# Optimization experiments

Hardware: AMD Instinct MI355X
Metric: run time of the kernel (lower is better)

Reference implementation:

```python
import jax, jax.numpy as jnp
import numpy as np

B, C_IN, L = 16, 64, 1024
HID, OUT, ORDER = 1024, 512, 4
EPS = 1e-5


def setup_inputs() -> dict:
    key = jax.random.key(0)
    ks = jax.random.split(key, 4)
    return {
        "x": jax.random.normal(ks[0], (B, C_IN, L), jnp.float32),
        "W_in": jax.random.normal(ks[1], (C_IN, HID), jnp.float32) / np.sqrt(C_IN).astype(np.float32),
        "b_in": jnp.zeros((HID,), jnp.float32),
        "coeffs1": jax.random.normal(ks[2], (HID, HID, ORDER), jnp.float32) * 0.01,
        "bias1": jnp.zeros((HID,), jnp.float32),
        "g1": jnp.ones((HID,), jnp.float32),
        "beta1": jnp.zeros((HID,), jnp.float32),
        "coeffs2": jax.random.normal(ks[3], (OUT, HID, ORDER), jnp.float32) * 0.01,
        "bias2": jnp.zeros((OUT,), jnp.float32),
        "g2": jnp.ones((OUT,), jnp.float32),
        "beta2": jnp.zeros((OUT,), jnp.float32),
    }


def _taylor_kan(x, coeffs, bias):
    # x: (B, L, C_in); coeffs: (out, C_in, order); y[b,l,o] = sum_i sum_c x^i * coeffs[o,c,i]
    # Expressed as order-wise GEMMs with a running power -- no (B,out,L,C) expand.
    order = coeffs.shape[-1]
    y = jnp.zeros(x.shape[:2] + (coeffs.shape[0],), x.dtype)
    xp = jnp.ones_like(x)  # x**0 (matches torch 0**0 == 1)
    for i in range(order):
        y = y + jnp.einsum('blc,oc->blo', xp, coeffs[:, :, i])
        if i + 1 < order:
            xp = xp * x
    return y + bias


def _layernorm(x, g, b):
    mu = jnp.mean(x, -1, keepdims=True)
    var = jnp.mean((x - mu) ** 2, -1, keepdims=True)
    return (x - mu) * jax.lax.rsqrt(var + EPS) * g + b


def reference(x, W_in, b_in, coeffs1, bias1, g1, beta1, coeffs2, bias2, g2, beta2):
    # x: (B, C_in, L) -> project channels to hidden: (B, L, HID)
    h = jnp.einsum('bcl,ch->blh', x, W_in) + b_in
    h = _taylor_kan(h, coeffs1, bias1)            # (B, L, HID)
    h = jax.nn.gelu(_layernorm(h, g1, beta1), approximate=False)
    h = _taylor_kan(h, coeffs2, bias2)            # (B, L, OUT)
    h = _layernorm(h, g2, beta2)
    return jnp.mean(h, axis=1)                    # adaptive avg pool over L -> (B, OUT)
```

## Files before the change

### kernel.cpp

```cpp
#include <hip/hip_runtime.h>
#include <math.h>

#define Bsz  16
#define CIN  64
#define LEN  1024
#define HIDN 1024
#define OUTN 512
#define MTOT (Bsz*LEN)
#define KTOT (3*HIDN)
#define LCHUNKS 32
#define LROWS   (LEN/LCHUNKS)

typedef __attribute__((ext_vector_type(8))) short bf16x8;
typedef __attribute__((ext_vector_type(16))) float f32x16;

__device__ __forceinline__ unsigned short f2bf(float x) {
    union { float f; unsigned int u; } v; v.f = x;
    unsigned int r = v.u + 0x7fff + ((v.u >> 16) & 1);
    return (unsigned short)(r >> 16);
}
__device__ __forceinline__ float bf2f(unsigned short u) {
    union { unsigned int u; float f; } v; v.u = ((unsigned int)u) << 16;
    return v.f;
}
__device__ __forceinline__ void gload_lds16(const void* g, void* l) {
    __builtin_amdgcn_global_load_lds((const __attribute__((address_space(1))) void*)g,
                                     (__attribute__((address_space(3))) void*)l, 16, 0, 0);
}

__global__ __launch_bounds__(256) void prep_all(const float* __restrict__ coeffs1,
                                                const float* __restrict__ bias1,
                                                const float* __restrict__ coeffs2,
                                                const float* __restrict__ bias2,
                                                const float* __restrict__ x,
                                                const float* __restrict__ Win,
                                                unsigned short* __restrict__ W1T,
                                                float* __restrict__ b1e,
                                                unsigned short* __restrict__ W2T,
                                                float* __restrict__ b2e,
                                                unsigned short* __restrict__ xT,
                                                unsigned short* __restrict__ WinT) {
    __shared__ float sm[64 * 65];
    int bid = blockIdx.x, t = threadIdx.x;
    if (bid < 1536) {
        const float* coeffs; const float* bias; unsigned short* WT; float* beff; int o;
        if (bid < 1024) { coeffs = coeffs1; bias = bias1; WT = W1T; beff = b1e; o = bid; }
        else            { coeffs = coeffs2; bias = bias2; WT = W2T; beff = b2e; o = bid - 1024; }
        float s = 0.f;
        unsigned short* wrow = WT + (size_t)o * KTOT;
        for (int c = t; c < HIDN; c += 256) {
            float4 v = *(const float4*)(coeffs + ((size_t)o * HIDN + c) * 4);
            s += v.x;
            wrow[c]            = f2bf(v.y);
            wrow[HIDN + c]     = f2bf(v.z);
            wrow[2 * HIDN + c] = f2bf(v.w);
        }
        for (int off = 32; off > 0; off >>= 1) s += __shfl_down(s, off, 64);
        if ((t & 63) == 0) sm[t >> 6] = s;
        __syncthreads();
        if (t == 0) beff[o] = bias[o] + sm[0] + sm[1] + sm[2] + sm[3];
    } else {
        const float* src; unsigned short* dstbase; size_t src_rstride;
        int c0;
        if (bid < 1792) {
            int tile = bid - 1536; int b = tile >> 4; c0 = (tile & 15) * 64;
            src = x + (size_t)b * CIN * LEN;  src_rstride = LEN;
            dstbase = xT + ((size_t)b * LEN + c0) * CIN;
        } else {
            int tile = bid - 1792; c0 = tile * 64;
            src = Win; src_rstride = HIDN;
            dstbase = WinT + (size_t)c0 * CIN;
        }
#pragma unroll
        for (int it = 0; it < 4; it++) {
            int idx = t + it * 256;
            int c = idx >> 4, q = idx & 15;
            float4 v = *(const float4*)(src + (size_t)c * src_rstride + c0 + q * 4);
            sm[c * 65 + q * 4 + 0] = v.x;
            sm[c * 65 + q * 4 + 1] = v.y;
            sm[c * 65 + q * 4 + 2] = v.z;
            sm[c * 65 + q * 4 + 3] = v.w;
        }
        __syncthreads();
        int ll = t >> 2, cg = (t & 3) * 16;
        unsigned short* dst = dstbase + (size_t)ll * CIN + cg;
#pragma unroll
        for (int j = 0; j < 4; j++) {
            int c = cg + j * 4;
            ushort4 w = { f2bf(sm[(c + 0) * 65 + ll]), f2bf(sm[(c + 1) * 65 + ll]),
                          f2bf(sm[(c + 2) * 65 + ll]), f2bf(sm[(c + 3) * 65 + ll]) };
            *(ushort4*)(dst + j * 4) = w;
        }
    }
}

__global__ __launch_bounds__(256) void proj_mfma(const unsigned short* __restrict__ xT,
                                                 const unsigned short* __restrict__ WinT,
                                                 const float* __restrict__ bin,
                                                 unsigned short* __restrict__ Hpow) {
    __shared__ unsigned short smem[2 * 128 * 64];
    unsigned short* As = smem;
    unsigned short* Bs = smem + 128 * 64;
    unsigned short* ht = smem;
    int t = threadIdx.x, lane = t & 63, wave = t >> 6;
    int m0 = blockIdx.x * 128, n0 = blockIdx.y * 128;
    int srow = lane >> 3, sgcc = (lane & 7) ^ srow;
    const unsigned short* Ab = xT + (size_t)m0 * CIN;
    const unsigned short* Bb = WinT + (size_t)n0 * CIN;

    f32x16 acc[2][2] = {};
    int wr = (wave >> 1) * 64, wc = (wave & 1) * 64;
    int row32 = lane & 31, half = lane >> 5;

#pragma unroll
    for (int j = 0; j < 4; j++) {
        int rgrp = wave * 32 + j * 8;
        gload_lds16(Ab + (size_t)(rgrp + srow) * CIN + sgcc * 8, As + rgrp * 64);
        gload_lds16(Bb + (size_t)(rgrp + srow) * CIN + sgcc * 8, Bs + rgrp * 64);
    }
    __syncthreads();
#pragma unroll
    for (int ks = 0; ks < 4; ks++) {
        int cidx = ks * 2 + half;
        bf16x8 af[2], bf[2];
#pragma unroll
        for (int mt = 0; mt < 2; mt++) {
            int r = wr + mt * 32 + row32;
            af[mt] = *(const bf16x8*)(As + r * 64 + ((cidx ^ (r & 7)) << 3));
        }
#pragma unroll
        for (int nt = 0; nt < 2; nt++) {
            int c = wc + nt * 32 + row32;
            bf[nt] = *(const bf16x8*)(Bs + c * 64 + ((cidx ^ (c & 7)) << 3));
        }
#pragma unroll
        for (int mt = 0; mt < 2; mt++)
#pragma unroll
            for (int nt = 0; nt < 2; nt++)
                acc[mt][nt] = __builtin_amdgcn_mfma_f32_32x32x16_bf16(af[mt], bf[nt], acc[mt][nt], 0, 0, 0);
    }
    __syncthreads();
#pragma unroll
    for (int nt = 0; nt < 2; nt++) {
        int ocl = wc + nt * 32 + row32;
        float bo = bin[n0 + ocl];
#pragma unroll
        for (int mt = 0; mt < 2; mt++) {
#pragma unroll
            for (int reg = 0; reg < 16; reg++) {
                int rl = wr + mt * 32 + (reg & 3) + 8 * (reg >> 2) + 4 * half;
                ht[rl * 128 + ocl] = f2bf(acc[mt][nt][reg] + bo);
            }
        }
    }
    __syncthreads();
#pragma unroll
    for (int p = 0; p < 8; p++) {
        int r = p * 16 + (t >> 4);
        int c = (t & 15) * 8;
        bf16x8 hv = *(const bf16x8*)(ht + r * 128 + c);
        bf16x8 h2v, h3v;
#pragma unroll
        for (int j = 0; j < 8; j++) {
            float f = bf2f((unsigned short)hv[j]);
            float f2 = f * f;
            h2v[j] = (short)f2bf(f2);
            h3v[j] = (short)f2bf(f2 * f);
        }
        unsigned short* d = Hpow + (size_t)(m0 + r) * KTOT + n0 + c;
        *(bf16x8*)(d)            = hv;
        *(bf16x8*)(d + HIDN)     = h2v;
        *(bf16x8*)(d + 2 * HIDN) = h3v;
    }
}

template<int N, bool BF16OUT>
__global__ __launch_bounds__(256) void mfma_gemm(const unsigned short* __restrict__ A,
                                                 const unsigned short* __restrict__ BT,
                                                 const float* __restrict__ beff,
                                                 void* __restrict__ Yv) {
    __shared__ unsigned short As[128 * 64];
    __shared__ unsigned short Bs[128 * 64];
    int t = threadIdx.x;
    int lane = t & 63, wave = t >> 6;
    int m0 = blockIdx.x * 128, n0 = blockIdx.y * 128;
    const unsigned short* Ab = A + (size_t)m0 * KTOT;
    const unsigned short* Bb = BT + (size_t)n0 * KTOT;

    int srow = lane >> 3;
    int sgcc = (lane & 7) ^ srow;

    f32x16 acc[2][2] = {};
    int wr = (wave >> 1) * 64;
    int wc = (wave & 1) * 64;
    int row32 = lane & 31, half = lane >> 5;

    for (int k0 = 0; k0 < KTOT; k0 += 64) {
#pragma unroll
        for (int j = 0; j < 4; j++) {
            int rgrp = wave * 32 + j * 8;
            gload_lds16(Ab + ((size_t)(rgrp + srow) * KTOT + k0 + sgcc * 8), As + rgrp * 64);
            gload_lds16(Bb + ((size_t)(rgrp + srow) * KTOT + k0 + sgcc * 8), Bs + rgrp * 64);
        }
        __syncthreads();
#pragma unroll
        for (int ks = 0; ks < 4; ks++) {
            int cidx = ks * 2 + half;
            bf16x8 af[2], bf[2];
#pragma unroll
            for (int mt = 0; mt < 2; mt++) {
                int r = wr + mt * 32 + row32;
                af[mt] = *(const bf16x8*)(As + r * 64 + ((cidx ^ (r & 7)) << 3));
            }
#pragma unroll
            for (int nt = 0; nt < 2; nt++) {
                int c = wc + nt * 32 + row32;
                bf[nt] = *(const bf16x8*)(Bs + c * 64 + ((cidx ^ (c & 7)) << 3));
            }
#pragma unroll
            for (int mt = 0; mt < 2; mt++)
#pragma unroll
                for (int nt = 0; nt < 2; nt++)
                    acc[mt][nt] = __builtin_amdgcn_mfma_f32_32x32x16_bf16(af[mt], bf[nt], acc[mt][nt], 0, 0, 0);
        }
        __syncthreads();
    }
#pragma unroll
    for (int nt = 0; nt < 2; nt++) {
        int oc = n0 + wc + nt * 32 + row32;
        float bo = beff[oc];
#pragma unroll
        for (int mt = 0; mt < 2; mt++) {
#pragma unroll
            for (int reg = 0; reg < 16; reg++) {
                int rl = (reg & 3) + 8 * (reg >> 2) + 4 * half;
                int mr = m0 + wr + mt * 32 + rl;
                float v = acc[mt][nt][reg] + bo;
                if (BF16OUT) ((unsigned short*)Yv)[(size_t)mr * N + oc] = f2bf(v);
                else         ((float*)Yv)[(size_t)mr * N + oc] = v;
            }
        }
    }
}

__global__ __launch_bounds__(256) void ln_gelu(const unsigned short* __restrict__ y1,
                                               const float* __restrict__ g,
                                               const float* __restrict__ be,
                                               unsigned short* __restrict__ Gpow) {
    __shared__ float2 red[2][2];
    int t = threadIdx.x;
    int rhalf = t >> 7, l = t & 127, wid = (t >> 6) & 1;
    int m = blockIdx.x * 2 + rhalf;
    bf16x8 u = *(const bf16x8*)(y1 + (size_t)m * HIDN + l * 8);
    float v[8];
    float s = 0.f, ss = 0.f;
#pragma unroll
    for (int j = 0; j < 8; j++) {
        v[j] = bf2f((unsigned short)u[j]);
        s += v[j]; ss += v[j] * v[j];
    }
    for (int off = 32; off > 0; off >>= 1) {
        s  += __shfl_down(s, off, 64);
        ss += __shfl_down(ss, off, 64);
    }
    if ((t & 63) == 0) red[rhalf][wid] = make_float2(s, ss);
    __syncthreads();
    float sT  = red[rhalf][0].x + red[rhalf][1].x;
    float ssT = red[rhalf][0].y + red[rhalf][1].y;
    float mu = sT * (1.f / HIDN);
    float var = ssT * (1.f / HIDN) - mu * mu;
    float rs = rsqrtf(var + 1e-5f);
    float4 gA = *(const float4*)(g + l * 8),  gB = *(const float4*)(g + l * 8 + 4);
    float4 bA = *(const float4*)(be + l * 8), bB = *(const float4*)(be + l * 8 + 4);
    float gv[8] = { gA.x, gA.y, gA.z, gA.w, gB.x, gB.y, gB.z, gB.w };
    float bv[8] = { bA.x, bA.y, bA.z, bA.w, bB.x, bB.y, bB.z, bB.w };
    bf16x8 p1, p2, p3;
#pragma unroll
    for (int j = 0; j < 8; j++) {
        float xn = (v[j] - mu) * rs * gv[j] + bv[j];
        float gl = xn * 0.5f * (1.f + erff(xn * 0.70710678118654752f));
        float g2 = gl * gl;
        p1[j] = (short)f2bf(gl);
        p2[j] = (short)f2bf(g2);
        p3[j] = (short)f2bf(g2 * gl);
    }
    unsigned short* dst = Gpow + (size_t)m * KTOT + l * 8;
    *(bf16x8*)(dst)            = p1;
    *(bf16x8*)(dst + HIDN)     = p2;
    *(bf16x8*)(dst + 2 * HIDN) = p3;
}

__global__ __launch_bounds__(256) void ln_pool_partial(const unsigned short* __restrict__ y2,
                                                       const float* __restrict__ g,
                                                       const float* __restrict__ be,
                                                       float* __restrict__ partial) {
    __shared__ float part[4][OUTN];
    int t = threadIdx.x, lane = t & 63, wave = t >> 6;
    int b = blockIdx.x, chunk = blockIdx.y;
    int mbase = b * LEN + chunk * LROWS;

    float4 gA = *(const float4*)(g + 8 * lane),  gB = *(const float4*)(g + 8 * lane + 4);
    float4 bA = *(const float4*)(be + 8 * lane), bB = *(const float4*)(be + 8 * lane + 4);
    float gv[8] = { gA.x, gA.y, gA.z, gA.w, gB.x, gB.y, gB.z, gB.w };
    float bv[8] = { bA.x, bA.y, bA.z, bA.w, bB.x, bB.y, bB.z, bB.w };

    float acc[8] = {0.f, 0.f, 0.f, 0.f, 0.f, 0.f, 0.f, 0.f};
    for (int rr = wave; rr < LROWS; rr += 4) {
        bf16x8 u = *(const bf16x8*)(y2 + (size_t)(mbase + rr) * OUTN + 8 * lane);
        float v[8];
        float s = 0.f, ss = 0.f;
#pragma unroll
        for (int j = 0; j < 8; j++) {
            v[j] = bf2f((unsigned short)u[j]);
            s += v[j]; ss += v[j] * v[j];
        }
        for (int off = 32; off > 0; off >>= 1) {
            s  += __shfl_down(s, off, 64);
            ss += __shfl_down(ss, off, 64);
        }
        s  = __shfl(s, 0, 64);
        ss = __shfl(ss, 0, 64);
        float mu = s * (1.f / OUTN);
        float var = ss * (1.f / OUTN) - mu * mu;
        float rs = rsqrtf(var + 1e-5f);
#pragma unroll
        for (int j = 0; j < 8; j++)
            acc[j] += (v[j] - mu) * rs * gv[j] + bv[j];
    }
    *(float4*)(&part[wave][8 * lane])     = *(float4*)(&acc[0]);
    *(float4*)(&part[wave][8 * lane + 4]) = *(float4*)(&acc[4]);
    __syncthreads();
    float p0 = part[0][2*t] + part[1][2*t] + part[2][2*t] + part[3][2*t];
    float p1 = part[0][2*t+1] + part[1][2*t+1] + part[2][2*t+1] + part[3][2*t+1];
    float* dst = partial + ((size_t)b * LCHUNKS + chunk) * OUTN;
    *(float2*)(dst + 2 * t) = make_float2(p0, p1);
}

__global__ __launch_bounds__(256) void pool_reduce(const float* __restrict__ partial,
                                                   float* __restrict__ out) {
    int b = blockIdx.x, t = threadIdx.x;
    const float* src = partial + (size_t)b * LCHUNKS * OUTN;
    float s0 = 0.f, s1 = 0.f;
    for (int c = 0; c < LCHUNKS; c++) {
        float2 v = *(const float2*)(src + (size_t)c * OUTN + 2 * t);
        s0 += v.x; s1 += v.y;
    }
    *(float2*)(out + (size_t)b * OUTN + 2 * t) = make_float2(s0 * (1.f / LEN), s1 * (1.f / LEN));
}

extern "C" void kernel_launch(void* const* d_in, const int* in_sizes, int n_in,
                              void* d_out, int out_size, void* d_ws, size_t ws_size,
                              hipStream_t stream) {
    const float* x       = (const float*)d_in[0];
    const float* Win     = (const float*)d_in[1];
    const float* bin     = (const float*)d_in[2];
    const float* coeffs1 = (const float*)d_in[3];
    const float* bias1   = (const float*)d_in[4];
    const float* g1      = (const float*)d_in[5];
    const float* beta1   = (const float*)d_in[6];
    const float* coeffs2 = (const float*)d_in[7];
    const float* bias2   = (const float*)d_in[8];
    const float* g2      = (const float*)d_in[9];
    const float* beta2   = (const float*)d_in[10];
    float* out = (float*)d_out;

    char* ws = (char*)d_ws;
    unsigned short* Hpow = (unsigned short*)ws;
    char* p1 = ws + (size_t)MTOT * KTOT * 2;
    unsigned short* y1   = (unsigned short*)p1;
    unsigned short* y2   = (unsigned short*)p1;
    char* p2 = p1 + (size_t)MTOT * HIDN * 2;
    unsigned short* W1T  = (unsigned short*)p2;
    char* p3 = p2 + (size_t)HIDN * KTOT * 2;
    unsigned short* W2T  = (unsigned short*)p3;
    char* p4 = p3 + (size_t)OUTN * KTOT * 2;
    float* b1e = (float*)p4;
    float* b2e = (float*)(p4 + HIDN * sizeof(float));
    char* p5 = p4 + (HIDN + OUTN) * sizeof(float);
    unsigned short* xT   = (unsigned short*)p5;
    char* p6 = p5 + (size_t)MTOT * CIN * 2;
    unsigned short* WinT = (unsigned short*)p6;
    unsigned short* G2pow = Hpow;
    float* partial = (float*)W1T;

    prep_all<<<1808, 256, 0, stream>>>(coeffs1, bias1, coeffs2, bias2, x, Win,
                                       W1T, b1e, W2T, b2e, xT, WinT);
    proj_mfma<<<dim3(MTOT / 128, HIDN / 128), 256, 0, stream>>>(xT, WinT, bin, Hpow);
    mfma_gemm<HIDN, true><<<dim3(MTOT / 128, HIDN / 128), 256, 0, stream>>>(Hpow, W1T, b1e, y1);
    ln_gelu<<<MTOT / 2, 256, 0, stream>>>(y1, g1, beta1, G2pow);
    mfma_gemm<OUTN, true><<<dim3(MTOT / 128, OUTN / 128), 256, 0, stream>>>(G2pow, W2T, b2e, y2);
    ln_pool_partial<<<dim3(Bsz, LCHUNKS), 256, 0, stream>>>(y2, g2, beta2, partial);
    pool_reduce<<<Bsz, 256, 0, stream>>>(partial, out);
}
```

Baseline: 313.2 us.

## Fold linear Taylor term of first KAN layer into input projection weights

Because h is linear in x, the order-1 term h·C1 equals x·(Win·C1) + bin·C1. The change precomputes Win·C1 (64 columns) and bin·C1 in a new kernel and appends x directly as the last 64 K-columns, shrinking the first GEMM's K from 3072 to 2112. It also stops writing the h term to the A buffer. The cost is an extra small kernel and slightly different rounding, since the folded weights are computed in fp32 from bf16 WinT and then rounded to bf16.

```diff
diff --git a/kernel.cpp b/kernel.cpp
--- a/kernel.cpp
+++ b/kernel.cpp
@@ -8,6 +8,7 @@
 #define OUTN 512
 #define MTOT (Bsz*LEN)
 #define KTOT (3*HIDN)
+#define KT1  (2*HIDN + CIN)
 #define LCHUNKS 32
 #define LROWS   (LEN/LCHUNKS)
 
@@ -42,14 +43,26 @@
                                                 unsigned short* __restrict__ WinT) {
     __shared__ float sm[64 * 65];
     int bid = blockIdx.x, t = threadIdx.x;
-    if (bid < 1536) {
-        const float* coeffs; const float* bias; unsigned short* WT; float* beff; int o;
-        if (bid < 1024) { coeffs = coeffs1; bias = bias1; WT = W1T; beff = b1e; o = bid; }
-        else            { coeffs = coeffs2; bias = bias2; WT = W2T; beff = b2e; o = bid - 1024; }
+    if (bid < 1024) {
+        int o = bid;
         float s = 0.f;
-        unsigned short* wrow = WT + (size_t)o * KTOT;
+        unsigned short* wrow = W1T + (size_t)o * KT1;
         for (int c = t; c < HIDN; c += 256) {
-            float4 v = *(const float4*)(coeffs + ((size_t)o * HIDN + c) * 4);
+            float4 v = *(const float4*)(coeffs1 + ((size_t)o * HIDN + c) * 4);
+            s += v.x;
+            wrow[c]        = f2bf(v.z);
+            wrow[HIDN + c] = f2bf(v.w);
+        }
+        for (int off = 32; off > 0; off >>= 1) s += __shfl_down(s, off, 64);
+        if ((t & 63) == 0) sm[t >> 6] = s;
+        __syncthreads();
+        if (t == 0) b1e[o] = bias1[o] + sm[0] + sm[1] + sm[2] + sm[3];
+    } else if (bid < 1536) {
+        int o = bid - 1024;
+        float s = 0.f;
+        unsigned short* wrow = W2T + (size_t)o * KTOT;
+        for (int c = t; c < HIDN; c += 256) {
+            float4 v = *(const float4*)(coeffs2 + ((size_t)o * HIDN + c) * 4);
             s += v.x;
             wrow[c]            = f2bf(v.y);
             wrow[HIDN + c]     = f2bf(v.z);
@@ -58,7 +71,7 @@
         for (int off = 32; off > 0; off >>= 1) s += __shfl_down(s, off, 64);
         if ((t & 63) == 0) sm[t >> 6] = s;
         __syncthreads();
-        if (t == 0) beff[o] = bias[o] + sm[0] + sm[1] + sm[2] + sm[3];
+        if (t == 0) b2e[o] = bias2[o] + sm[0] + sm[1] + sm[2] + sm[3];
     } else {
         const float* src; unsigned short* dstbase; size_t src_rstride;
         int c0;
@@ -94,10 +107,39 @@
     }
 }
 
+__global__ __launch_bounds__(256) void wc1_kernel(const float* __restrict__ coeffs1,
+                                                  const unsigned short* __restrict__ WinT,
+                                                  const float* __restrict__ bin,
+                                                  unsigned short* __restrict__ W1T,
+                                                  float* __restrict__ b1e) {
+    __shared__ float c1s[HIDN];
+    __shared__ float part[4][64];
+    __shared__ float pbred[4];
+    int o = blockIdx.x, t = threadIdx.x, lane = t & 63, wave = t >> 6;
+    for (int c = t; c < HIDN; c += 256)
+        c1s[c] = coeffs1[((size_t)o * HIDN + c) * 4 + 1];
+    __syncthreads();
+    float acc = 0.f;
+    int cbase = wave * 256;
+    for (int c = cbase; c < cbase + 256; c++)
+        acc += bf2f(WinT[c * CIN + lane]) * c1s[c];
+    part[wave][lane] = acc;
+    float pb = 0.f;
+    for (int c = t; c < HIDN; c += 256) pb += bin[c] * c1s[c];
+    for (int off = 32; off > 0; off >>= 1) pb += __shfl_down(pb, off, 64);
+    if (lane == 0) pbred[wave] = pb;
+    __syncthreads();
+    if (t < 64) {
+        float v = part[0][t] + part[1][t] + part[2][t] + part[3][t];
+        W1T[(size_t)o * KT1 + 2 * HIDN + t] = f2bf(v);
+    }
+    if (t == 0) b1e[o] += pbred[0] + pbred[1] + pbred[2] + pbred[3];
+}
+
 __global__ __launch_bounds__(256) void proj_mfma(const unsigned short* __restrict__ xT,
                                                  const unsigned short* __restrict__ WinT,
                                                  const float* __restrict__ bin,
-                                                 unsigned short* __restrict__ Hpow) {
+                                                 unsigned short* __restrict__ A1) {
     __shared__ unsigned short smem[2 * 128 * 64];
     unsigned short* As = smem;
     unsigned short* Bs = smem + 128 * 64;
@@ -167,14 +209,22 @@
             h2v[j] = (short)f2bf(f2);
             h3v[j] = (short)f2bf(f2 * f);
         }
-        unsigned short* d = Hpow + (size_t)(m0 + r) * KTOT + n0 + c;
-        *(bf16x8*)(d)            = hv;
-        *(bf16x8*)(d + HIDN)     = h2v;
-        *(bf16x8*)(d + 2 * HIDN) = h3v;
-    }
-}
-
-template<int N, bool BF16OUT>
+        unsigned short* d = A1 + (size_t)(m0 + r) * KT1 + n0 + c;
+        *(bf16x8*)(d)        = h2v;
+        *(bf16x8*)(d + HIDN) = h3v;
+    }
+    if (n0 == 0) {
+#pragma unroll
+        for (int it = 0; it < 4; it++) {
+            int idx = t + it * 256;
+            int r = idx >> 3, cc = (idx & 7) * 8;
+            bf16x8 v = *(const bf16x8*)(xT + (size_t)(m0 + r) * CIN + cc);
+            *(bf16x8*)(A1 + (size_t)(m0 + r) * KT1 + 2 * HIDN + cc) = v;
+        }
+    }
+}
+
+template<int N, int KT, bool BF16OUT>
 __global__ __launch_bounds__(256) void mfma_gemm(const unsigned short* __restrict__ A,
                                                  const unsigned short* __restrict__ BT,
                                                  const float* __restrict__ beff,
@@ -184,8 +234,8 @@
     int t = threadIdx.x;
     int lane = t & 63, wave = t >> 6;
     int m0 = blockIdx.x * 128, n0 = blockIdx.y * 128;
-    const unsigned short* Ab = A + (size_t)m0 * KTOT;
-    const unsigned short* Bb = BT + (size_t)n0 * KTOT;
+    const unsigned short* Ab = A + (size_t)m0 * KT;
+    const unsigned short* Bb = BT + (size_t)n0 * KT;
 
     int srow = lane >> 3;
     int sgcc = (lane & 7) ^ srow;
@@ -195,12 +245,12 @@
     int wc = (wave & 1) * 64;
     int row32 = lane & 31, half = lane >> 5;
 
-    for (int k0 = 0; k0 < KTOT; k0 += 64) {
+    for (int k0 = 0; k0 < KT; k0 += 64) {
 #pragma unroll
         for (int j = 0; j < 4; j++) {
             int rgrp = wave * 32 + j * 8;
-            gload_lds16(Ab + ((size_t)(rgrp + srow) * KTOT + k0 + sgcc * 8), As + rgrp * 64);
-            gload_lds16(Bb + ((size_t)(rgrp + srow) * KTOT + k0 + sgcc * 8), Bs + rgrp * 64);
+            gload_lds16(Ab + ((size_t)(rgrp + srow) * KT + k0 + sgcc * 8), As + rgrp * 64);
+            gload_lds16(Bb + ((size_t)(rgrp + srow) * KT + k0 + sgcc * 8), Bs + rgrp * 64);
         }
         __syncthreads();
 #pragma unroll
@@ -365,13 +415,14 @@
     float* out = (float*)d_out;
 
     char* ws = (char*)d_ws;
-    unsigned short* Hpow = (unsigned short*)ws;
+    unsigned short* A1   = (unsigned short*)ws;
+    unsigned short* Gpow = (unsigned short*)ws;
     char* p1 = ws + (size_t)MTOT * KTOT * 2;
     unsigned short* y1   = (unsigned short*)p1;
     unsigned short* y2   = (unsigned short*)p1;
     char* p2 = p1 + (size_t)MTOT * HIDN * 2;
     unsigned short* W1T  = (unsigned short*)p2;
-    char* p3 = p2 + (size_t)HIDN * KTOT * 2;
+    char* p3 = p2 + (size_t)HIDN * KT1 * 2;
     unsigned short* W2T  = (unsigned short*)p3;
     char* p4 = p3 + (size_t)OUTN * KTOT * 2;
     float* b1e = (float*)p4;
@@ -380,15 +431,15 @@
     unsigned short* xT   = (unsigned short*)p5;
     char* p6 = p5 + (size_t)MTOT * CIN * 2;
     unsigned short* WinT = (unsigned short*)p6;
-    unsigned short* G2pow = Hpow;
     float* partial = (float*)W1T;
 
     prep_all<<<1808, 256, 0, stream>>>(coeffs1, bias1, coeffs2, bias2, x, Win,
                                        W1T, b1e, W2T, b2e, xT, WinT);
-    proj_mfma<<<dim3(MTOT / 128, HIDN / 128), 256, 0, stream>>>(xT, WinT, bin, Hpow);
-    mfma_gemm<HIDN, true><<<dim3(MTOT / 128, HIDN / 128), 256, 0, stream>>>(Hpow, W1T, b1e, y1);
-    ln_gelu<<<MTOT / 2, 256, 0, stream>>>(y1, g1, beta1, G2pow);
-    mfma_gemm<OUTN, true><<<dim3(MTOT / 128, OUTN / 128), 256, 0, stream>>>(G2pow, W2T, b2e, y2);
+    wc1_kernel<<<HIDN, 256, 0, stream>>>(coeffs1, WinT, bin, W1T, b1e);
+    proj_mfma<<<dim3(MTOT / 128, HIDN / 128), 256, 0, stream>>>(xT, WinT, bin, A1);
+    mfma_gemm<HIDN, KT1, true><<<dim3(MTOT / 128, HIDN / 128), 256, 0, stream>>>(A1, W1T, b1e, y1);
+    ln_gelu<<<MTOT / 2, 256, 0, stream>>>(y1, g1, beta1, Gpow);
+    mfma_gemm<OUTN, KTOT, true><<<dim3(MTOT / 128, OUTN / 128), 256, 0, stream>>>(Gpow, W2T, b2e, y2);
     ln_pool_partial<<<dim3(Bsz, LCHUNKS), 256, 0, stream>>>(y2, g2, beta2, partial);
     pool_reduce<<<Bsz, 256, 0, stream>>>(partial, out);
 }
```

Result: faster. 288.9 us (-7.8%).
